# Kernel tuning notes

Hardware: AMD Instinct MI355X
Metric: run time of the kernel (lower is better)

The kernel has to match this reference:

```python
import jax, jax.numpy as jnp
import numpy as np

ALPHA = 1.0   # alpha=1 -> loss = alpha*loss_shape; temporal term weighted by (1-alpha)=0
GAMMA = 0.01  # soft-DTW smoothing
G = 0.05      # logistic weight steepness (weighted-DTW, Jeong et al. 2011)
BIG = 1e9     # finite 'infinity' (keeps vjp NaN-free vs. true inf)


def _softdtw(D, gamma):
    # Soft-DTW value of cost matrix D [N,N] via anti-diagonal (wavefront) scan.
    # R(i,j) = D[i,j] + softmin_gamma(R(i-1,j-1), R(i-1,j), R(i,j-1)),
    # R(-1,-1)=0, other out-of-range = +inf. Diagonal k holds cells (i, k-i).
    N = D.shape[-1]
    i = jnp.arange(N)

    def step(carry, k):
        r2, r1 = carry            # diagonals k-2 and k-1, indexed by row i
        j = k - i
        valid = (j >= 0) & (j < N)
        dk = jnp.where(valid, D[i, jnp.clip(j, 0, N - 1)], 0.0)
        up = jnp.where(i > 0, jnp.roll(r1, 1), BIG)     # R(i-1, j)
        left = r1                                        # R(i, j-1) (BIG where invalid)
        dg = jnp.where(i > 0, jnp.roll(r2, 1), BIG)      # R(i-1, j-1)
        dg = jnp.where((i == 0) & (j == 0), 0.0, dg)     # R(-1,-1) = 0 boundary
        smin = -gamma * jax.nn.logsumexp(jnp.stack([-dg, -up, -left]) / gamma, axis=0)
        rk = jnp.where(valid, dk + smin, BIG)
        return (r1, rk), None

    r0 = jnp.full((N,), BIG, dtype=D.dtype)
    (_, rlast), _ = jax.lax.scan(step, (r0, r0), jnp.arange(2 * N - 1))
    return rlast[N - 1]  # cell (N-1, N-1)


def _weighted_dilate(inp, tgt):
    B, N, _ = inp.shape
    idx = jnp.arange(N, dtype=inp.dtype)
    # modified-logistic weight on |i-j|, midpoint N/2, steepness g
    w = 1.0 / (1.0 + jnp.exp(-G * (jnp.abs(idx[:, None] - idx[None, :]) - N / 2.0)))
    # pairwise squared euclidean cost: D[b,i,j] = sum_d (tgt[b,i,d]-inp[b,j,d])^2
    D = jnp.sum((tgt[:, :, None, :] - inp[:, None, :, :]) ** 2, axis=-1) * w
    sdtw = jax.vmap(lambda d: _softdtw(d, GAMMA))(D)  # [B]
    loss_shape = jnp.mean(sdtw)
    return ALPHA * loss_shape  # (1-alpha)*loss_temporal == 0 at default alpha=1


def setup_inputs() -> dict:
    key = jax.random.key(0)
    k1, k2 = jax.random.split(key)
    B, N, Dm = 32, 1024, 1
    return {
        "input": jax.random.normal(k1, (B, N, Dm), dtype=jnp.float32),
        "target": jax.random.normal(k2, (B, N, Dm), dtype=jnp.float32),
    }


def reference(input, target):
    return _weighted_dilate(input, target)
```

## Files before the change

kernel.cpp:

```cpp
#include <hip/hip_runtime.h>
#include <math.h>

#define NN 1024
#define BATCH 32
#define P 8
#define NW 4
#define THREADS 256
#define DD 32
#define SW 32
#define SPAN 160
#define NT 64
#define RB 2
#define WLN 2368
#define GW 0.05f
#define K2 144.2695040888963f
#define INV_K2 0.0069314718055994531f
#define BIGS 1.4426950408889634e11f

#define EXP2F(x) __builtin_amdgcn_exp2f(x)
#define LOG2F(x) __builtin_amdgcn_logf(x)

typedef unsigned long long u64;

__device__ __forceinline__ float dppshr(float oldv, float src) {
    return __int_as_float(__builtin_amdgcn_update_dpp(
        __float_as_int(oldv), __float_as_int(src), 0x138, 0xF, 0xF, false));
}

__device__ __forceinline__ u64 pk(float v, unsigned tag) {
    return ((u64)tag << 32) | (u64)__float_as_uint(v);
}

__global__ __launch_bounds__(256) void ws_init(int* __restrict__ acks,
                                               u64* __restrict__ gx) {
    if (blockIdx.x == 128) acks[threadIdx.x] = 0;
    else gx[(size_t)blockIdx.x * 256 + threadIdx.x] = 0;
}

#define STEPBODY(d, DOMASK) do {                                              \
        xv = dppshr(((d) == 0) ? xf0 : xv, xv);        \
        const float up = dppshr(((d) == 0) ? bndUp : r1, r1);  \
        const float dg = dgp;                                                 \
        const float left = r1;                                                \
        const float diff = ti - xv;                                           \
        const float dk = diff * diff * wreg[(d)];         \
        const float mn = fminf(fminf(dg, up), left);                          \
        const float md = __builtin_amdgcn_fmed3f(dg, up, left);               \
        const float mx = fmaxf(fmaxf(dg, up), left);                          \
        const float ss = 1.0f + EXP2F(mn - md) + EXP2F(mn - mx);              \
        float r = dk + mn - LOG2F(ss);                                        \
        if (DOMASK) r = (jj0 >= -(d)) ? r : BIGS;        \
        r2 = r1; r1 = r; dgp = up;                                            \
    } while (0)

__global__ __launch_bounds__(THREADS) void sdtw_pipe8(
        const float* __restrict__ inp, const float* __restrict__ tgt,
        float* __restrict__ partial, int* __restrict__ acks,
        u64* __restrict__ gx)
{
    __shared__ __align__(16) float xs[NN];
    __shared__ __align__(16) float wlu[WLN];
    __shared__ float2 exch[2][SPAN];

    const int bid = blockIdx.x;
    const int b = bid & 31;
    const int p = bid >> 5;
    const int tid = threadIdx.x;
    const int w = tid >> 6;
    const int lane = tid & 63;

    const int mlo = 767 - 256 * p;
    for (int tdx = tid; tdx < NN; tdx += THREADS)
        xs[tdx] = inp[b * NN + tdx];
    for (int tdx = tid; tdx < WLN; tdx += THREADS) {
        int m = tdx + mlo;
        float val = K2;
        if ((unsigned)m <= 2046u)
            val = K2 / (1.0f + __expf(-GW * (fabsf((float)m - 1023.0f) - 512.0f)));
        wlu[tdx] = val;
    }

    const int i = 128 * p - (DD - 1) + SW * w + lane;
    const int i0 = i - lane;
    const bool rowValid = (unsigned)i < (unsigned)NN;
    int ic = min(max(i, 0), NN - 1);
    const float ti = tgt[b * NN + ic];
    const int imask = rowValid ? i : 0x3FFFFFFF;
    const int wq = 256 + 256 * p - 2 * i;

    float r1 = BIGS, r2 = BIGS;
    float dgp = (i == 0) ? 0.0f : BIGS;
    float bndUp = BIGS;
    float xv = 0.0f;
    int ackC = 0;

    __syncthreads();

    const int fin = b * P + p;
    const int fout = fin + 1;
    u64* gout = gx + (size_t)fout * (RB * DD * 2);
    u64* ginb = gx + (size_t)fin * (RB * DD * 2);

    const bool isProd = (w == NW - 1) && (p < P - 1);
    const bool isCons = (w == 0) && (p > 0);

    u64 pfA = 0, pfB = 0, pfC0 = 0, pfC1 = 0;

    int cP  = min(max(-1 - i, 0), NN - 1);
    int c0P = min(max(-i0, 0), NN - 1);
    float xpreA = xs[cP];
    float xpreB = xs[c0P];

    for (int t = 0; t < NT; ++t) {
        if (t > 0) {
            if (isProd) {
                if (t > RB) {
                    while (ackC < t - RB) {
                        __builtin_amdgcn_s_sleep(1);
                        ackC = __hip_atomic_load(&acks[fout], __ATOMIC_RELAXED,
                                                 __HIP_MEMORY_SCOPE_AGENT);
                    }
                }
                if (lane >= DD - 1 && lane < 63) {
                    u64* gq = gout + (size_t)((t - 1) & (RB - 1)) * (DD * 2)
                                   + (size_t)(lane - (DD - 1)) * 2;
                    __hip_atomic_store(&gq[0], pk(r1, (unsigned)t),
                                       __ATOMIC_RELAXED, __HIP_MEMORY_SCOPE_AGENT);
                    __hip_atomic_store(&gq[1], pk(r2, (unsigned)t),
                                       __ATOMIC_RELAXED, __HIP_MEMORY_SCOPE_AGENT);
                }
                ackC = __hip_atomic_load(&acks[fout], __ATOMIC_RELAXED,
                                         __HIP_MEMORY_SCOPE_AGENT);
            }
            if (w > 0) {
                const int buf = (t - 1) & 1;
                if (lane < DD - 1) { float2 vv = exch[buf][SW * w + lane]; r1 = vv.x; r2 = vv.y; }
                float2 bv = exch[buf][SW * w - 1];
                float nd = dppshr(0.0f, r2);
                if (lane == 0)           { bndUp = bv.x; dgp = bv.y; }
                else if (lane <= DD - 2) dgp = nd;
            } else if (p > 0) {
                const unsigned expect = (unsigned)t;
                const u64* gslot = ginb + (size_t)((t - 1) & (RB - 1)) * (DD * 2);
                for (;;) {
                    int ok = 1;
                    if (lane < DD - 1)
                        ok = ((unsigned)(pfA >> 32) == expect) &
                             ((unsigned)(pfB >> 32) == expect);
                    if (lane == 0)
                        ok &= ((unsigned)(pfC0 >> 32) == expect) &
                              ((unsigned)(pfC1 >> 32) == expect);
                    if (__all(ok)) break;
                    if (lane < DD - 1) {
                        pfA = __hip_atomic_load((u64*)&gslot[(size_t)(lane + 1) * 2],
                                                __ATOMIC_RELAXED, __HIP_MEMORY_SCOPE_AGENT);
                        pfB = __hip_atomic_load((u64*)&gslot[(size_t)(lane + 1) * 2 + 1],
                                                __ATOMIC_RELAXED, __HIP_MEMORY_SCOPE_AGENT);
                    }
                    if (lane == 0) {
                        pfC0 = __hip_atomic_load((u64*)&gslot[0],
                                                 __ATOMIC_RELAXED, __HIP_MEMORY_SCOPE_AGENT);
                        pfC1 = __hip_atomic_load((u64*)&gslot[1],
                                                 __ATOMIC_RELAXED, __HIP_MEMORY_SCOPE_AGENT);
                    }
                }
                if (lane < DD - 1) { r1 = __uint_as_float((unsigned)pfA);
                                     r2 = __uint_as_float((unsigned)pfB); }
                float nd = dppshr(0.0f, r2);
                if (lane == 0) { bndUp = __uint_as_float((unsigned)pfC0);
                                 dgp   = __uint_as_float((unsigned)pfC1); }
                else if (lane <= DD - 2) dgp = nd;
                if (lane == 0)
                    __hip_atomic_store(&acks[fin], (int)(pfC0 >> 32),
                                       __ATOMIC_RELAXED, __HIP_MEMORY_SCOPE_AGENT);
            } else {
                bndUp = BIGS;
            }
        }

        const int kbase = t << 5;
        const int jj0 = kbase - imask;

        const float* wp = &wlu[kbase + wq];
        float wreg[DD];
        #pragma unroll
        for (int h = 0; h < DD / 2; ++h) {
            float2 w2 = *reinterpret_cast<const float2*>(&wp[2 * h]);
            wreg[2 * h] = w2.x; wreg[2 * h + 1] = w2.y;
        }

        const float xf0 = xpreB;
        xv = xpreA;
        { int cN  = min(max(kbase + DD - 1 - i, 0), NN - 1);
          int c0N = min(max(kbase + DD - i0, 0), NN - 1);
          xpreA = xs[cN]; xpreB = xs[c0N]; }

        if (i0 >= 0 && kbase >= i0 + 63) {
            #pragma unroll
            for (int d = 0; d < DD; ++d) STEPBODY(d, 0);
        } else {
            #pragma unroll
            for (int d = 0; d < DD; ++d) STEPBODY(d, 1);
        }
        if (t == NT - 1) break;

        if (w < NW - 1 && lane >= DD - 1)
            exch[t & 1][SW * w + lane] = make_float2(r1, r2);

        if (isCons) {
            const u64* gslot = ginb + (size_t)(t & (RB - 1)) * (DD * 2);
            if (lane < DD - 1) {
                pfA = __hip_atomic_load((u64*)&gslot[(size_t)(lane + 1) * 2],
                                        __ATOMIC_RELAXED, __HIP_MEMORY_SCOPE_AGENT);
                pfB = __hip_atomic_load((u64*)&gslot[(size_t)(lane + 1) * 2 + 1],
                                        __ATOMIC_RELAXED, __HIP_MEMORY_SCOPE_AGENT);
            }
            if (lane == 0) {
                pfC0 = __hip_atomic_load((u64*)&gslot[0],
                                         __ATOMIC_RELAXED, __HIP_MEMORY_SCOPE_AGENT);
                pfC1 = __hip_atomic_load((u64*)&gslot[1],
                                         __ATOMIC_RELAXED, __HIP_MEMORY_SCOPE_AGENT);
            }
        }

        asm volatile("s_waitcnt lgkmcnt(0)" ::: "memory");
        __builtin_amdgcn_s_barrier();
        asm volatile("" ::: "memory");
        __builtin_amdgcn_sched_barrier(0);
    }

    if (i == NN - 1) partial[b] = r2 * INV_K2;
}

__global__ __launch_bounds__(64) void reduce_mean32(const float* __restrict__ partial,
                                                    float* __restrict__ out) {
    float v = (threadIdx.x < BATCH) ? partial[threadIdx.x] : 0.0f;
    #pragma unroll
    for (int off = 32; off > 0; off >>= 1) v += __shfl_down(v, off);
    if (threadIdx.x == 0) out[0] = v * (1.0f / (float)BATCH);
}

extern "C" void kernel_launch(void* const* d_in, const int* in_sizes, int n_in,
                              void* d_out, int out_size, void* d_ws, size_t ws_size,
                              hipStream_t stream) {
    const float* inp = (const float*)d_in[0];
    const float* tgt = (const float*)d_in[1];
    float* out = (float*)d_out;

    float* partial = (float*)d_ws;
    int* acks  = (int*)((char*)d_ws + 128);
    u64* gx    = (u64*)((char*)d_ws + 2048);

    ws_init<<<129, 256, 0, stream>>>(acks, gx);
    sdtw_pipe8<<<BATCH * P, THREADS, 0, stream>>>(inp, tgt, partial, acks, gx);
    reduce_mean32<<<1, 64, 0, stream>>>(partial, out);
}
```

Before: 205.3 us.

## Split each batch row into 16 row-stripes, one wave per batch

```diff
diff --git a/kernel.cpp b/kernel.cpp
--- a/kernel.cpp
+++ b/kernel.cpp
@@ -3,15 +3,14 @@
 
 #define NN 1024
 #define BATCH 32
-#define P 8
-#define NW 4
+#define P 16
+#define NWB 4
 #define THREADS 256
+#define NBLK 128
 #define DD 32
-#define SW 32
-#define SPAN 160
 #define NT 64
-#define RB 2
-#define WLN 2368
+#define RB 4
+#define WLN 2176
 #define GW 0.05f
 #define K2 144.2695040888963f
 #define INV_K2 0.0069314718055994531f
@@ -33,15 +32,16 @@
 
 __global__ __launch_bounds__(256) void ws_init(int* __restrict__ acks,
                                                u64* __restrict__ gx) {
-    if (blockIdx.x == 128) acks[threadIdx.x] = 0;
-    else gx[(size_t)blockIdx.x * 256 + threadIdx.x] = 0;
+    const int bid = blockIdx.x;
+    if (bid < 256) gx[(size_t)bid * 256 + threadIdx.x] = 0;
+    else acks[(bid - 256) * 256 + threadIdx.x] = 0;
 }
 
 #define STEPBODY(d, DOMASK) do {                                              \
-        xv = dppshr(((d) == 0) ? xf0 : xv, xv);        \
-        const float up = dppshr(((d) == 0) ? bndUp : r1, r1);  \
-        const float dg = dgp;                                                 \
-        const float left = r1;                                                \
+        xv = dppshr(xin[(d)], xv);                     \
+        const float up = dppshr(bnd1, r1);                    \
+        const float dg = dgp;                                 \
+        const float left = r1;                                \
         const float diff = ti - xv;                                           \
         const float dk = diff * diff * wreg[(d)];         \
         const float mn = fminf(fminf(dg, up), left);                          \
@@ -50,28 +50,31 @@
         const float ss = 1.0f + EXP2F(mn - md) + EXP2F(mn - mx);              \
         float r = dk + mn - LOG2F(ss);                                        \
         if (DOMASK) r = (jj0 >= -(d)) ? r : BIGS;        \
-        r2 = r1; r1 = r; dgp = up;                                            \
+        r2 = r1; r1 = r; dgp = up; bnd1 = bd[(d)];                            \
+        *(float*)((char*)wptr + (wmsk & (unsigned)((d) * 4))) = r1;           \
     } while (0)
 
-__global__ __launch_bounds__(THREADS) void sdtw_pipe8(
+__global__ __launch_bounds__(THREADS) void sdtw_pipe16(
         const float* __restrict__ inp, const float* __restrict__ tgt,
         float* __restrict__ partial, int* __restrict__ acks,
         u64* __restrict__ gx)
 {
-    __shared__ __align__(16) float xs[NN];
+    __shared__ __align__(16) float xs[NWB][NN];
     __shared__ __align__(16) float wlu[WLN];
-    __shared__ float2 exch[2][SPAN];
+    __shared__ __align__(16) float pub[NWB][DD];
+    __shared__ __align__(16) float barr[NWB][DD];
+    __shared__ float dmp[NWB][64];
 
     const int bid = blockIdx.x;
-    const int b = bid & 31;
-    const int p = bid >> 5;
+    const int g = bid & 7;
+    const int p = bid >> 3;
     const int tid = threadIdx.x;
     const int w = tid >> 6;
     const int lane = tid & 63;
-
-    const int mlo = 767 - 256 * p;
-    for (int tdx = tid; tdx < NN; tdx += THREADS)
-        xs[tdx] = inp[b * NN + tdx];
+    const int b = g + 8 * w;
+
+    for (int idx = lane; idx < NN; idx += 64) xs[w][idx] = inp[b * NN + idx];
+    const int mlo = 895 - 128 * p;
     for (int tdx = tid; tdx < WLN; tdx += THREADS) {
         int m = tdx + mlo;
         float val = K2;
@@ -80,17 +83,13 @@
         wlu[tdx] = val;
     }
 
-    const int i = 128 * p - (DD - 1) + SW * w + lane;
-    const int i0 = i - lane;
-    const bool rowValid = (unsigned)i < (unsigned)NN;
-    int ic = min(max(i, 0), NN - 1);
-    const float ti = tgt[b * NN + ic];
-    const int imask = rowValid ? i : 0x3FFFFFFF;
-    const int wq = 256 + 256 * p - 2 * i;
+    const int i = 64 * p + lane;
+    const float ti = tgt[b * NN + i];
+    const float* xb = xs[w];
 
     float r1 = BIGS, r2 = BIGS;
     float dgp = (i == 0) ? 0.0f : BIGS;
-    float bndUp = BIGS;
+    float bnd1 = BIGS;
     float xv = 0.0f;
     int ackC = 0;
 
@@ -98,138 +97,114 @@
 
     const int fin = b * P + p;
     const int fout = fin + 1;
-    u64* gout = gx + (size_t)fout * (RB * DD * 2);
-    u64* ginb = gx + (size_t)fin * (RB * DD * 2);
-
-    const bool isProd = (w == NW - 1) && (p < P - 1);
-    const bool isCons = (w == 0) && (p > 0);
-
-    u64 pfA = 0, pfB = 0, pfC0 = 0, pfC1 = 0;
-
-    int cP  = min(max(-1 - i, 0), NN - 1);
-    int c0P = min(max(-i0, 0), NN - 1);
-    float xpreA = xs[cP];
-    float xpreB = xs[c0P];
-
-    for (int t = 0; t < NT; ++t) {
-        if (t > 0) {
-            if (isProd) {
-                if (t > RB) {
-                    while (ackC < t - RB) {
-                        __builtin_amdgcn_s_sleep(1);
-                        ackC = __hip_atomic_load(&acks[fout], __ATOMIC_RELAXED,
-                                                 __HIP_MEMORY_SCOPE_AGENT);
-                    }
-                }
-                if (lane >= DD - 1 && lane < 63) {
-                    u64* gq = gout + (size_t)((t - 1) & (RB - 1)) * (DD * 2)
-                                   + (size_t)(lane - (DD - 1)) * 2;
-                    __hip_atomic_store(&gq[0], pk(r1, (unsigned)t),
-                                       __ATOMIC_RELAXED, __HIP_MEMORY_SCOPE_AGENT);
-                    __hip_atomic_store(&gq[1], pk(r2, (unsigned)t),
-                                       __ATOMIC_RELAXED, __HIP_MEMORY_SCOPE_AGENT);
-                }
-                ackC = __hip_atomic_load(&acks[fout], __ATOMIC_RELAXED,
-                                         __HIP_MEMORY_SCOPE_AGENT);
-            }
-            if (w > 0) {
-                const int buf = (t - 1) & 1;
-                if (lane < DD - 1) { float2 vv = exch[buf][SW * w + lane]; r1 = vv.x; r2 = vv.y; }
-                float2 bv = exch[buf][SW * w - 1];
-                float nd = dppshr(0.0f, r2);
-                if (lane == 0)           { bndUp = bv.x; dgp = bv.y; }
-                else if (lane <= DD - 2) dgp = nd;
-            } else if (p > 0) {
-                const unsigned expect = (unsigned)t;
-                const u64* gslot = ginb + (size_t)((t - 1) & (RB - 1)) * (DD * 2);
-                for (;;) {
-                    int ok = 1;
-                    if (lane < DD - 1)
-                        ok = ((unsigned)(pfA >> 32) == expect) &
-                             ((unsigned)(pfB >> 32) == expect);
-                    if (lane == 0)
-                        ok &= ((unsigned)(pfC0 >> 32) == expect) &
-                              ((unsigned)(pfC1 >> 32) == expect);
-                    if (__all(ok)) break;
-                    if (lane < DD - 1) {
-                        pfA = __hip_atomic_load((u64*)&gslot[(size_t)(lane + 1) * 2],
-                                                __ATOMIC_RELAXED, __HIP_MEMORY_SCOPE_AGENT);
-                        pfB = __hip_atomic_load((u64*)&gslot[(size_t)(lane + 1) * 2 + 1],
-                                                __ATOMIC_RELAXED, __HIP_MEMORY_SCOPE_AGENT);
-                    }
-                    if (lane == 0) {
-                        pfC0 = __hip_atomic_load((u64*)&gslot[0],
-                                                 __ATOMIC_RELAXED, __HIP_MEMORY_SCOPE_AGENT);
-                        pfC1 = __hip_atomic_load((u64*)&gslot[1],
-                                                 __ATOMIC_RELAXED, __HIP_MEMORY_SCOPE_AGENT);
-                    }
-                }
-                if (lane < DD - 1) { r1 = __uint_as_float((unsigned)pfA);
-                                     r2 = __uint_as_float((unsigned)pfB); }
-                float nd = dppshr(0.0f, r2);
-                if (lane == 0) { bndUp = __uint_as_float((unsigned)pfC0);
-                                 dgp   = __uint_as_float((unsigned)pfC1); }
-                else if (lane <= DD - 2) dgp = nd;
-                if (lane == 0)
-                    __hip_atomic_store(&acks[fin], (int)(pfC0 >> 32),
-                                       __ATOMIC_RELAXED, __HIP_MEMORY_SCOPE_AGENT);
-            } else {
-                bndUp = BIGS;
-            }
-        }
-
-        const int kbase = t << 5;
-        const int jj0 = kbase - imask;
-
-        const float* wp = &wlu[kbase + wq];
-        float wreg[DD];
+    u64* gout = gx + (size_t)fout * (RB * DD);
+    const u64* ginb = gx + (size_t)fin * (RB * DD);
+    const bool prod = (p < P - 1);
+    const bool cons = (p > 0);
+
+    float* wptr = (lane == 63) ? &pub[w][0] : &dmp[w][lane];
+    const unsigned wmsk = (lane == 63) ? ~0u : 0u;
+
+    u64 pf = 0;
+    if (cons && lane < DD)
+        pf = __hip_atomic_load(&ginb[lane], __ATOMIC_RELAXED,
+                               __HIP_MEMORY_SCOPE_AGENT);
+
+    float wreg[DD], xin[DD], bd[DD];
+    {
+        const float* wp = &wlu[128 - 2 * lane];
         #pragma unroll
         for (int h = 0; h < DD / 2; ++h) {
             float2 w2 = *reinterpret_cast<const float2*>(&wp[2 * h]);
             wreg[2 * h] = w2.x; wreg[2 * h + 1] = w2.y;
         }
-
-        const float xf0 = xpreB;
-        xv = xpreA;
-        { int cN  = min(max(kbase + DD - 1 - i, 0), NN - 1);
-          int c0N = min(max(kbase + DD - i0, 0), NN - 1);
-          xpreA = xs[cN]; xpreB = xs[c0N]; }
-
-        if (i0 >= 0 && kbase >= i0 + 63) {
+        #pragma unroll
+        for (int h = 0; h < DD / 4; ++h) {
+            float4 q = *reinterpret_cast<const float4*>(&xb[4 * h]);
+            xin[4 * h] = q.x; xin[4 * h + 1] = q.y;
+            xin[4 * h + 2] = q.z; xin[4 * h + 3] = q.w;
+        }
+    }
+
+    for (int t = 0; t < NT; ++t) {
+        const int kbase = t << 5;
+
+        if (cons) {
+            const u64* gslot = ginb + (size_t)(t & (RB - 1)) * DD;
+            const unsigned expect = (unsigned)(t + 1);
+            for (;;) {
+                int ok = (lane < DD) ? ((unsigned)(pf >> 32) == expect) : 1;
+                if (__all(ok)) break;
+                if (lane < DD)
+                    pf = __hip_atomic_load(&gslot[lane], __ATOMIC_RELAXED,
+                                           __HIP_MEMORY_SCOPE_AGENT);
+            }
+            if (lane < DD) barr[w][lane] = __uint_as_float((unsigned)pf);
+            if (lane == 0)
+                __hip_atomic_store(&acks[fin], t + 1, __ATOMIC_RELAXED,
+                                   __HIP_MEMORY_SCOPE_AGENT);
+            #pragma unroll
+            for (int h = 0; h < DD / 4; ++h) {
+                float4 q = *reinterpret_cast<const float4*>(&barr[w][4 * h]);
+                bd[4 * h] = q.x; bd[4 * h + 1] = q.y;
+                bd[4 * h + 2] = q.z; bd[4 * h + 3] = q.w;
+            }
+        } else {
+            #pragma unroll
+            for (int d = 0; d < DD; ++d) bd[d] = BIGS;
+        }
+
+        const int jj0 = kbase - i;
+        if (kbase >= 64 * p + 63) {
             #pragma unroll
             for (int d = 0; d < DD; ++d) STEPBODY(d, 0);
         } else {
             #pragma unroll
             for (int d = 0; d < DD; ++d) STEPBODY(d, 1);
         }
+
+        if (prod) {
+            float bv = (lane < DD) ? pub[w][lane] : 0.0f;
+            if (t >= RB) {
+                while (ackC < t - (RB - 1)) {
+                    __builtin_amdgcn_s_sleep(1);
+                    ackC = __hip_atomic_load(&acks[fout], __ATOMIC_RELAXED,
+                                             __HIP_MEMORY_SCOPE_AGENT);
+                }
+            }
+            if (lane < DD)
+                __hip_atomic_store(&gout[(size_t)(t & (RB - 1)) * DD + lane],
+                                   pk(bv, (unsigned)(t + 1)),
+                                   __ATOMIC_RELAXED, __HIP_MEMORY_SCOPE_AGENT);
+            ackC = __hip_atomic_load(&acks[fout], __ATOMIC_RELAXED,
+                                     __HIP_MEMORY_SCOPE_AGENT);
+        }
         if (t == NT - 1) break;
 
-        if (w < NW - 1 && lane >= DD - 1)
-            exch[t & 1][SW * w + lane] = make_float2(r1, r2);
-
-        if (isCons) {
-            const u64* gslot = ginb + (size_t)(t & (RB - 1)) * (DD * 2);
-            if (lane < DD - 1) {
-                pfA = __hip_atomic_load((u64*)&gslot[(size_t)(lane + 1) * 2],
-                                        __ATOMIC_RELAXED, __HIP_MEMORY_SCOPE_AGENT);
-                pfB = __hip_atomic_load((u64*)&gslot[(size_t)(lane + 1) * 2 + 1],
-                                        __ATOMIC_RELAXED, __HIP_MEMORY_SCOPE_AGENT);
-            }
-            if (lane == 0) {
-                pfC0 = __hip_atomic_load((u64*)&gslot[0],
-                                         __ATOMIC_RELAXED, __HIP_MEMORY_SCOPE_AGENT);
-                pfC1 = __hip_atomic_load((u64*)&gslot[1],
-                                         __ATOMIC_RELAXED, __HIP_MEMORY_SCOPE_AGENT);
-            }
-        }
-
-        asm volatile("s_waitcnt lgkmcnt(0)" ::: "memory");
-        __builtin_amdgcn_s_barrier();
-        asm volatile("" ::: "memory");
-        __builtin_amdgcn_sched_barrier(0);
+        if (cons && lane < DD)
+            pf = __hip_atomic_load(&ginb[(size_t)((t + 1) & (RB - 1)) * DD + lane],
+                                   __ATOMIC_RELAXED, __HIP_MEMORY_SCOPE_AGENT);
+
+        {
+            const int kn = kbase + DD;
+            const float* wp = &wlu[kn + 128 - 2 * lane];
+            #pragma unroll
+            for (int h = 0; h < DD / 2; ++h) {
+                float2 w2 = *reinterpret_cast<const float2*>(&wp[2 * h]);
+                wreg[2 * h] = w2.x; wreg[2 * h + 1] = w2.y;
+            }
+            int jb = kn - 64 * p;
+            int base = min(max(jb, 0), NN - DD);
+            #pragma unroll
+            for (int h = 0; h < DD / 4; ++h) {
+                float4 q = *reinterpret_cast<const float4*>(&xb[base + 4 * h]);
+                xin[4 * h] = q.x; xin[4 * h + 1] = q.y;
+                xin[4 * h + 2] = q.z; xin[4 * h + 3] = q.w;
+            }
+        }
     }
 
-    if (i == NN - 1) partial[b] = r2 * INV_K2;
+    if (p == P - 1 && lane == 63) partial[b] = r2 * INV_K2;
 }
 
 __global__ __launch_bounds__(64) void reduce_mean32(const float* __restrict__ partial,
@@ -249,9 +224,9 @@
 
     float* partial = (float*)d_ws;
     int* acks  = (int*)((char*)d_ws + 128);
-    u64* gx    = (u64*)((char*)d_ws + 2048);
-
-    ws_init<<<129, 256, 0, stream>>>(acks, gx);
-    sdtw_pipe8<<<BATCH * P, THREADS, 0, stream>>>(inp, tgt, partial, acks, gx);
+    u64* gx    = (u64*)((char*)d_ws + 128 + 2048);
+
+    ws_init<<<258, 256, 0, stream>>>(acks, gx);
+    sdtw_pipe16<<<NBLK, THREADS, 0, stream>>>(inp, tgt, partial, acks, gx);
     reduce_mean32<<<1, 64, 0, stream>>>(partial, out);
 }
```

After: 285.8 us. +39.2%, slower.

## Batch inter-block boundary handoff over two steps with a deeper ring buffer

Applied to the files above, without the earlier changes.

```diff
diff --git a/kernel.cpp b/kernel.cpp
--- a/kernel.cpp
+++ b/kernel.cpp
@@ -10,7 +10,7 @@
 #define SW 32
 #define SPAN 160
 #define NT 64
-#define RB 2
+#define RB 4
 #define WLN 2368
 #define GW 0.05f
 #define K2 144.2695040888963f
@@ -33,7 +33,7 @@
 
 __global__ __launch_bounds__(256) void ws_init(int* __restrict__ acks,
                                                u64* __restrict__ gx) {
-    if (blockIdx.x == 128) acks[threadIdx.x] = 0;
+    if (blockIdx.x == 512) acks[threadIdx.x] = 0;
     else gx[(size_t)blockIdx.x * 256 + threadIdx.x] = 0;
 }
 
@@ -92,19 +92,22 @@
     float dgp = (i == 0) ? 0.0f : BIGS;
     float bndUp = BIGS;
     float xv = 0.0f;
+    float bf1 = BIGS, bf2 = BIGS;
     int ackC = 0;
 
     __syncthreads();
 
     const int fin = b * P + p;
     const int fout = fin + 1;
-    u64* gout = gx + (size_t)fout * (RB * DD * 2);
-    u64* ginb = gx + (size_t)fin * (RB * DD * 2);
+    u64* gout = gx + (size_t)fout * (RB * DD * 4);
+    const u64* ginb = gx + (size_t)fin * (RB * DD * 4);
 
     const bool isProd = (w == NW - 1) && (p < P - 1);
     const bool isCons = (w == 0) && (p > 0);
 
-    u64 pfA = 0, pfB = 0, pfC0 = 0, pfC1 = 0;
+    u64 pfa = 0, pfb = 0, pfc = 0, pfd = 0;
+    u64 pba = 0, pbb = 0, pbc = 0, pbd = 0;
+    float nr1 = 0.0f, nr2 = 0.0f, nbx = 0.0f, nby = 0.0f;
 
     int cP  = min(max(-1 - i, 0), NN - 1);
     int c0P = min(max(-i0, 0), NN - 1);
@@ -114,23 +117,33 @@
     for (int t = 0; t < NT; ++t) {
         if (t > 0) {
             if (isProd) {
-                if (t > RB) {
-                    while (ackC < t - RB) {
-                        __builtin_amdgcn_s_sleep(1);
-                        ackC = __hip_atomic_load(&acks[fout], __ATOMIC_RELAXED,
-                                                 __HIP_MEMORY_SCOPE_AGENT);
-                    }
+                if (t & 1) { bf1 = r1; bf2 = r2; }
+                const bool doPub = (!(t & 1) && t >= 2) || (t == NT - 1);
+                if (doPub) {
+                    const int pr = ((t & 1) ? (t - 1) : (t - 2)) >> 1;
+                    if (pr >= RB) {
+                        while (ackC < pr + 1 - RB) {
+                            __builtin_amdgcn_s_sleep(1);
+                            ackC = __hip_atomic_load(&acks[fout], __ATOMIC_RELAXED,
+                                                     __HIP_MEMORY_SCOPE_AGENT);
+                        }
+                    }
+                    if (lane >= DD - 1 && lane < 63) {
+                        u64* gq = gout + (size_t)(pr & (RB - 1)) * (DD * 4)
+                                       + (size_t)(lane - (DD - 1)) * 4;
+                        const unsigned tg = (unsigned)(pr + 1);
+                        __hip_atomic_store(&gq[0], pk(bf1, tg),
+                                           __ATOMIC_RELAXED, __HIP_MEMORY_SCOPE_AGENT);
+                        __hip_atomic_store(&gq[1], pk(bf2, tg),
+                                           __ATOMIC_RELAXED, __HIP_MEMORY_SCOPE_AGENT);
+                        __hip_atomic_store(&gq[2], pk(r1, tg),
+                                           __ATOMIC_RELAXED, __HIP_MEMORY_SCOPE_AGENT);
+                        __hip_atomic_store(&gq[3], pk(r2, tg),
+                                           __ATOMIC_RELAXED, __HIP_MEMORY_SCOPE_AGENT);
+                    }
+                    ackC = __hip_atomic_load(&acks[fout], __ATOMIC_RELAXED,
+                                             __HIP_MEMORY_SCOPE_AGENT);
                 }
-                if (lane >= DD - 1 && lane < 63) {
-                    u64* gq = gout + (size_t)((t - 1) & (RB - 1)) * (DD * 2)
-                                   + (size_t)(lane - (DD - 1)) * 2;
-                    __hip_atomic_store(&gq[0], pk(r1, (unsigned)t),
-                                       __ATOMIC_RELAXED, __HIP_MEMORY_SCOPE_AGENT);
-                    __hip_atomic_store(&gq[1], pk(r2, (unsigned)t),
-                                       __ATOMIC_RELAXED, __HIP_MEMORY_SCOPE_AGENT);
-                }
-                ackC = __hip_atomic_load(&acks[fout], __ATOMIC_RELAXED,
-                                         __HIP_MEMORY_SCOPE_AGENT);
             }
             if (w > 0) {
                 const int buf = (t - 1) & 1;
@@ -140,39 +153,59 @@
                 if (lane == 0)           { bndUp = bv.x; dgp = bv.y; }
                 else if (lane <= DD - 2) dgp = nd;
             } else if (p > 0) {
-                const unsigned expect = (unsigned)t;
-                const u64* gslot = ginb + (size_t)((t - 1) & (RB - 1)) * (DD * 2);
-                for (;;) {
-                    int ok = 1;
-                    if (lane < DD - 1)
-                        ok = ((unsigned)(pfA >> 32) == expect) &
-                             ((unsigned)(pfB >> 32) == expect);
+                if (t & 1) {
+                    const int pr = (t - 1) >> 1;
+                    const unsigned expect = (unsigned)(pr + 1);
+                    const u64* gslot = ginb + (size_t)(pr & (RB - 1)) * (DD * 4);
+                    for (;;) {
+                        int ok = 1;
+                        if (lane < DD - 1)
+                            ok = ((unsigned)(pfa >> 32) == expect) &
+                                 ((unsigned)(pfb >> 32) == expect) &
+                                 ((unsigned)(pfc >> 32) == expect) &
+                                 ((unsigned)(pfd >> 32) == expect);
+                        if (lane == 0)
+                            ok &= ((unsigned)(pba >> 32) == expect) &
+                                  ((unsigned)(pbb >> 32) == expect) &
+                                  ((unsigned)(pbc >> 32) == expect) &
+                                  ((unsigned)(pbd >> 32) == expect);
+                        if (__all(ok)) break;
+                        if (lane < DD - 1) {
+                            const u64* q = &gslot[(size_t)(lane + 1) * 4];
+                            pfa = __hip_atomic_load(&q[0], __ATOMIC_RELAXED, __HIP_MEMORY_SCOPE_AGENT);
+                            pfb = __hip_atomic_load(&q[1], __ATOMIC_RELAXED, __HIP_MEMORY_SCOPE_AGENT);
+                            pfc = __hip_atomic_load(&q[2], __ATOMIC_RELAXED, __HIP_MEMORY_SCOPE_AGENT);
+                            pfd = __hip_atomic_load(&q[3], __ATOMIC_RELAXED, __HIP_MEMORY_SCOPE_AGENT);
+                        }
+                        if (lane == 0) {
+                            pba = __hip_atomic_load(&gslot[0], __ATOMIC_RELAXED, __HIP_MEMORY_SCOPE_AGENT);
+                            pbb = __hip_atomic_load(&gslot[1], __ATOMIC_RELAXED, __HIP_MEMORY_SCOPE_AGENT);
+                            pbc = __hip_atomic_load(&gslot[2], __ATOMIC_RELAXED, __HIP_MEMORY_SCOPE_AGENT);
+                            pbd = __hip_atomic_load(&gslot[3], __ATOMIC_RELAXED, __HIP_MEMORY_SCOPE_AGENT);
+                        }
+                    }
+                    if (lane < DD - 1) {
+                        r1 = __uint_as_float((unsigned)pfa);
+                        r2 = __uint_as_float((unsigned)pfb);
+                        nr1 = __uint_as_float((unsigned)pfc);
+                        nr2 = __uint_as_float((unsigned)pfd);
+                    }
+                    float nd = dppshr(0.0f, r2);
+                    if (lane == 0) {
+                        bndUp = __uint_as_float((unsigned)pba);
+                        dgp   = __uint_as_float((unsigned)pbb);
+                        nbx   = __uint_as_float((unsigned)pbc);
+                        nby   = __uint_as_float((unsigned)pbd);
+                    } else if (lane <= DD - 2) dgp = nd;
                     if (lane == 0)
-                        ok &= ((unsigned)(pfC0 >> 32) == expect) &
-                              ((unsigned)(pfC1 >> 32) == expect);
-                    if (__all(ok)) break;
-                    if (lane < DD - 1) {
-                        pfA = __hip_atomic_load((u64*)&gslot[(size_t)(lane + 1) * 2],
-                                                __ATOMIC_RELAXED, __HIP_MEMORY_SCOPE_AGENT);
-                        pfB = __hip_atomic_load((u64*)&gslot[(size_t)(lane + 1) * 2 + 1],
-                                                __ATOMIC_RELAXED, __HIP_MEMORY_SCOPE_AGENT);
-                    }
-                    if (lane == 0) {
-                        pfC0 = __hip_atomic_load((u64*)&gslot[0],
-                                                 __ATOMIC_RELAXED, __HIP_MEMORY_SCOPE_AGENT);
-                        pfC1 = __hip_atomic_load((u64*)&gslot[1],
-                                                 __ATOMIC_RELAXED, __HIP_MEMORY_SCOPE_AGENT);
-                    }
+                        __hip_atomic_store(&acks[fin], (int)(pba >> 32),
+                                           __ATOMIC_RELAXED, __HIP_MEMORY_SCOPE_AGENT);
+                } else {
+                    if (lane < DD - 1) { r1 = nr1; r2 = nr2; }
+                    float nd = dppshr(0.0f, r2);
+                    if (lane == 0)           { bndUp = nbx; dgp = nby; }
+                    else if (lane <= DD - 2) dgp = nd;
                 }
-                if (lane < DD - 1) { r1 = __uint_as_float((unsigned)pfA);
-                                     r2 = __uint_as_float((unsigned)pfB); }
-                float nd = dppshr(0.0f, r2);
-                if (lane == 0) { bndUp = __uint_as_float((unsigned)pfC0);
-                                 dgp   = __uint_as_float((unsigned)pfC1); }
-                else if (lane <= DD - 2) dgp = nd;
-                if (lane == 0)
-                    __hip_atomic_store(&acks[fin], (int)(pfC0 >> 32),
-                                       __ATOMIC_RELAXED, __HIP_MEMORY_SCOPE_AGENT);
             } else {
                 bndUp = BIGS;
             }
@@ -207,19 +240,21 @@
         if (w < NW - 1 && lane >= DD - 1)
             exch[t & 1][SW * w + lane] = make_float2(r1, r2);
 
-        if (isCons) {
-            const u64* gslot = ginb + (size_t)(t & (RB - 1)) * (DD * 2);
+        if (isCons && !(t & 1)) {
+            const int pr = t >> 1;
+            const u64* gslot = ginb + (size_t)(pr & (RB - 1)) * (DD * 4);
             if (lane < DD - 1) {
-                pfA = __hip_atomic_load((u64*)&gslot[(size_t)(lane + 1) * 2],
-                                        __ATOMIC_RELAXED, __HIP_MEMORY_SCOPE_AGENT);
-                pfB = __hip_atomic_load((u64*)&gslot[(size_t)(lane + 1) * 2 + 1],
-                                        __ATOMIC_RELAXED, __HIP_MEMORY_SCOPE_AGENT);
+                const u64* q = &gslot[(size_t)(lane + 1) * 4];
+                pfa = __hip_atomic_load(&q[0], __ATOMIC_RELAXED, __HIP_MEMORY_SCOPE_AGENT);
+                pfb = __hip_atomic_load(&q[1], __ATOMIC_RELAXED, __HIP_MEMORY_SCOPE_AGENT);
+                pfc = __hip_atomic_load(&q[2], __ATOMIC_RELAXED, __HIP_MEMORY_SCOPE_AGENT);
+                pfd = __hip_atomic_load(&q[3], __ATOMIC_RELAXED, __HIP_MEMORY_SCOPE_AGENT);
             }
             if (lane == 0) {
-                pfC0 = __hip_atomic_load((u64*)&gslot[0],
-                                         __ATOMIC_RELAXED, __HIP_MEMORY_SCOPE_AGENT);
-                pfC1 = __hip_atomic_load((u64*)&gslot[1],
-                                         __ATOMIC_RELAXED, __HIP_MEMORY_SCOPE_AGENT);
+                pba = __hip_atomic_load(&gslot[0], __ATOMIC_RELAXED, __HIP_MEMORY_SCOPE_AGENT);
+                pbb = __hip_atomic_load(&gslot[1], __ATOMIC_RELAXED, __HIP_MEMORY_SCOPE_AGENT);
+                pbc = __hip_atomic_load(&gslot[2], __ATOMIC_RELAXED, __HIP_MEMORY_SCOPE_AGENT);
+                pbd = __hip_atomic_load(&gslot[3], __ATOMIC_RELAXED, __HIP_MEMORY_SCOPE_AGENT);
             }
         }
 
@@ -251,7 +286,7 @@
     int* acks  = (int*)((char*)d_ws + 128);
     u64* gx    = (u64*)((char*)d_ws + 2048);
 
-    ws_init<<<129, 256, 0, stream>>>(acks, gx);
+    ws_init<<<513, 256, 0, stream>>>(acks, gx);
     sdtw_pipe8<<<BATCH * P, THREADS, 0, stream>>>(inp, tgt, partial, acks, gx);
     reduce_mean32<<<1, 64, 0, stream>>>(partial, out);
 }
```

After: 205.2 us, median of 2. Within noise of the previous version (-0.1%).
